# Optimization experiments

Measured on AMD Instinct MI355X. Metric: run time of the kernel, lower is better.

Reference implementation:

```python
import jax, jax.numpy as jnp
import numpy as np

B, H, NC, CS, D = 4, 16, 64, 64, 64
BASE_LR = 1.0
EPS = 1e-6


def setup_inputs() -> dict:
    key = jax.random.key(0)
    ks = jax.random.split(key, 4)
    xk = jax.random.normal(ks[0], (B, H, NC, CS, D), jnp.float32)
    xv = jax.random.normal(ks[1], (B, H, NC, CS, D), jnp.float32)
    # weights/theta use the module's N(0, 0.02) init scale
    weight = 0.02 * jax.random.normal(ks[2], (H, D, D), jnp.float32)
    bias = jnp.zeros((H, 1, D), jnp.float32)
    gamma = jnp.ones((H, 1, D), jnp.float32)
    beta = jnp.zeros((H, 1, D), jnp.float32)
    theta = 0.02 * jax.random.normal(ks[3], (H, D, 1), jnp.float32)
    theta_bias = jnp.zeros((H, 1, 1), jnp.float32)
    alpha = jnp.zeros((CS,), jnp.float32)
    return dict(xk=xk, xv=xv, weight=weight, bias=bias, gamma=gamma,
                beta=beta, theta=theta, theta_bias=theta_bias, alpha=alpha)


def _ttt(xk, xv, weight, bias, gamma, beta, theta, theta_bias, alpha):
    Bq, Hq, NCq, CSq, Dq = xk.shape
    # TTTDynamicLearningGate: token_idx = clamp(1/arange + alpha, 0)
    token_idx = jnp.maximum(1.0 / jnp.arange(1, CSq + 1, dtype=xk.dtype) + alpha, 0.0)
    token_eta = token_idx[None, None, :, None]  # [1,1,CS,1]
    g = gamma[None]       # [1,H,1,D]
    bt = beta[None]       # [1,H,1,D]
    tb = theta_bias[None]  # [1,H,1,1]
    # detach(): tile slow weights over batch -> fast weights
    W0 = jnp.broadcast_to(weight[None], (Bq, Hq, Dq, Dq))
    b0 = jnp.broadcast_to(bias[None], (Bq, Hq, 1, Dq))

    def step(carry, chunk):
        W, b = carry
        xk_c, xv_c = chunk  # [B,H,CS,D]
        # lr gate: eta = token_eta * (base_lr * sigmoid(x @ theta + b) / head_dim)
        lr = jax.nn.sigmoid(jnp.einsum('bhkc,hcd->bhkd', xk_c, theta) + tb)
        eta = token_eta * (BASE_LR * lr / Dq)  # [B,H,CS,1]
        # forward through fast weights (depth = 1)
        z = xk_c @ W + b
        # multi-head LayerNorm, detailed
        mu = z.mean(-1, keepdims=True)
        var = ((z - mu) ** 2).mean(-1, keepdims=True)
        std = jnp.sqrt(var + EPS)
        x_hat = (z - mu) / std
        y = g * x_hat + bt
        # L2 reconstruction grad through LN (manual backward)
        grad_out = y - (xv_c - xk_c)
        gxh = grad_out * g
        grad_x = (Dq * gxh - gxh.sum(-1, keepdims=True)
                  - x_hat * (gxh * x_hat).sum(-1, keepdims=True)) / (Dq * std)
        # fast-weight delta + step()
        dW = jnp.einsum('bhkd,bhke->bhde', eta * xk_c, grad_x)
        db = (eta * grad_x).sum(-2, keepdims=True)
        Wn, bn = W - dW, b - db
        return (Wn, bn), xk_c @ Wn + bn

    chunks = (jnp.moveaxis(xk, 2, 0), jnp.moveaxis(xv, 2, 0))  # [NC,B,H,CS,D]
    (_, _), outs = jax.lax.scan(step, (W0, b0), chunks)
    return jnp.moveaxis(outs, 0, 2)  # [B,H,NC,CS,D]


def reference(xk, xv, weight, bias, gamma, beta, theta, theta_bias, alpha):
    return _ttt(xk, xv, weight, bias, gamma, beta, theta, theta_bias, alpha)
```

## Files before the change

kernel.cpp:

```cpp
#include <hip/hip_runtime.h>
#include <hip/hip_bf16.h>
#include <math.h>

#define NCC 64
#define CSC 64
#define DC 64
#define S 72
#define SZ 68
#define EPSF 1e-6f
#define LDS_BYTES 82944

typedef __attribute__((ext_vector_type(8))) short bf16x8;
typedef __attribute__((ext_vector_type(4))) float f32x4;
typedef __attribute__((ext_vector_type(4))) short short4v;

static __device__ __forceinline__ short cvt_bf16(float x) {
    union { __hip_bfloat16 b; short s; } u;
    u.b = __float2bfloat16(x);
    return u.s;
}

#define DPP_ROR_ADD(v, N)                                                     \
    do {                                                                      \
        union { float f; int i; } _u, _r;                                     \
        _u.f = (v);                                                           \
        _r.i = __builtin_amdgcn_mov_dpp(_u.i, 0x120 + (N), 0xF, 0xF, true);   \
        (v) += _r.f;                                                          \
    } while (0)

static __device__ __forceinline__ float red16(float v) {
    DPP_ROR_ADD(v, 1);
    DPP_ROR_ADD(v, 2);
    DPP_ROR_ADD(v, 4);
    DPP_ROR_ADD(v, 8);
    return v;
}

__global__ __launch_bounds__(512, 1) void ttt_kernel(
    const float* __restrict__ xk, const float* __restrict__ xv,
    const float* __restrict__ weight, const float* __restrict__ bias,
    const float* __restrict__ gamma, const float* __restrict__ beta,
    const float* __restrict__ theta, const float* __restrict__ theta_bias,
    const float* __restrict__ alpha, float* __restrict__ out)
{
    extern __shared__ char sb[];
    auto xs_rm = (short (*)[CSC][S])(sb);
    auto xsT   = (short (*)[DC][S]) (sb + 18432);
    auto gsT   = (short (*)[S])     (sb + 36864);
    auto Gr    = (short (*)[S])     (sb + 46080);
    auto Wtb   = (short (*)[S])     (sb + 55296);
    auto zT    = (float (*)[SZ])    (sb + 64512);
    auto dbp   = (float (*)[DC])    (sb + 81920);

    const int t  = threadIdx.x;
    const int w  = t >> 6;
    const bool lo = (w < 4);
    const int ws = w & 3;
    const int l  = t & 63;
    const int g  = l >> 4, la = l & 15;
    const int r0 = 16*ws + 4*g;
    const int ts = 64*ws + l;
    const int bh = blockIdx.x;
    const int h  = bh & 15;

    const size_t bh_off = (size_t)bh * NCC*CSC*DC;
    const float* xkb = xk + bh_off;
    const float* xvb = xv + bh_off;
    float*       ob  = out + bh_off;

    float bcol[4];
#pragma unroll
    for (int n = 0; n < 4; ++n) bcol[n] = bias[h*DC + 16*n + la];

    float gam[4], bet[4], thv[4], tok[4], tb = 0.f;
    float Wreg[4][4];
    float xkg[4][4], xvg[4][4];
    float4 xl[4];
    float xkh[4][4];

    if (lo) {
#pragma unroll
        for (int n = 0; n < 4; ++n) {
            gam[n] = gamma[h*DC + 16*n + la];
            bet[n] = beta [h*DC + 16*n + la];
            thv[n] = theta[h*DC + 16*n + la];
        }
        tb = theta_bias[h];
#pragma unroll
        for (int i = 0; i < 4; ++i)
            tok[i] = fmaxf(1.0f/(float)(r0+i+1) + alpha[r0+i], 0.0f);
        const float* wg = weight + h*DC*DC;
#pragma unroll
        for (int i = 0; i < 4; ++i)
#pragma unroll
            for (int n = 0; n < 4; ++n)
                Wreg[i][n] = wg[(r0+i)*DC + 16*n + la];
#pragma unroll
        for (int n = 0; n < 4; ++n) {
            short4v sv;
#pragma unroll
            for (int i = 0; i < 4; ++i) sv[i] = cvt_bf16(Wreg[i][n]);
            *(short4v*)&Wtb[16*n + la][r0] = sv;
        }
#pragma unroll
        for (int i = 0; i < 4; ++i)
#pragma unroll
            for (int n = 0; n < 4; ++n) {
                xkg[i][n] = xkb[(r0+i)*DC + 16*n + la];
                xvg[i][n] = xvb[(r0+i)*DC + 16*n + la];
            }
    } else {
#pragma unroll
        for (int i4 = 0; i4 < 4; ++i4) xl[i4] = ((const float4*)xkb)[ts + 256*i4];
#pragma unroll
        for (int i = 0; i < 4; ++i)
#pragma unroll
            for (int n = 0; n < 4; ++n)
                xkh[i][n] = xkb[(r0+i)*DC + 16*n + la];
#pragma unroll
        for (int i4 = 0; i4 < 4; ++i4) {
            int f = ts + 256*i4, k = f >> 4, j = f & 15;
            short4v s4;
            s4[0]=cvt_bf16(xl[i4].x); s4[1]=cvt_bf16(xl[i4].y);
            s4[2]=cvt_bf16(xl[i4].z); s4[3]=cvt_bf16(xl[i4].w);
            *(short4v*)&xs_rm[0][k][4*j] = s4;
        }
#pragma unroll
        for (int n = 0; n < 4; ++n) {
            short4v sv;
#pragma unroll
            for (int i = 0; i < 4; ++i) sv[i] = cvt_bf16(xkh[i][n]);
            *(short4v*)&xsT[0][16*n + la][r0] = sv;
        }
    }
    __syncthreads();

    for (int c = 0; c < NCC; ++c) {
        const int cb = c & 1, nb = cb ^ 1;

        if (lo) {
            const bf16x8 a0 = *(const bf16x8*)&xs_rm[cb][16*ws + la][8*g];
            const bf16x8 a1 = *(const bf16x8*)&xs_rm[cb][16*ws + la][32 + 8*g];
            f32x4 zt[4];
#pragma unroll
            for (int n = 0; n < 4; ++n) {
                bf16x8 w0 = *(const bf16x8*)&Wtb[16*n + la][8*g];
                bf16x8 w1 = *(const bf16x8*)&Wtb[16*n + la][32 + 8*g];
                f32x4 zz = {0.f,0.f,0.f,0.f};
                zz = __builtin_amdgcn_mfma_f32_16x16x32_bf16(a0, w0, zz, 0,0,0);
                zz = __builtin_amdgcn_mfma_f32_16x16x32_bf16(a1, w1, zz, 0,0,0);
                zt[n] = zz;
                *(f32x4*)&zT[16*n + la][r0] = zz;
            }
            float gsv[4][4];
#pragma unroll
            for (int i = 0; i < 4; ++i) {
                float z0 = zt[0][i]+bcol[0], z1 = zt[1][i]+bcol[1];
                float z2 = zt[2][i]+bcol[2], z3 = zt[3][i]+bcol[3];
                float szz = red16(z0*z0 + z1*z1 + z2*z2 + z3*z3);
                float sz  = red16(z0 + z1 + z2 + z3);
                float thd = red16(xkg[i][0]*thv[0] + xkg[i][1]*thv[1] +
                                  xkg[i][2]*thv[2] + xkg[i][3]*thv[3]);
                float mu  = sz * (1.0f/DC);
                float var = szz*(1.0f/DC) - mu*mu;
                float rstd = rsqrtf(var + EPSF);
                float ex  = __expf(-(thd + tb));
                float lr  = __builtin_amdgcn_rcpf(1.0f + ex);
                float eta = tok[i]*lr*(1.0f/DC);
                float zz4[4] = {z0,z1,z2,z3};
                float xh[4], gxh[4], a1v = 0.f, a2v = 0.f;
#pragma unroll
                for (int n = 0; n < 4; ++n) {
                    xh[n] = (zz4[n]-mu)*rstd;
                    float y  = fmaf(gam[n], xh[n], bet[n]);
                    float go = y - xvg[i][n] + xkg[i][n];
                    gxh[n] = go*gam[n];
                    a1v += gxh[n];
                    a2v = fmaf(gxh[n], xh[n], a2v);
                }
                float s1 = red16(a1v), s2 = red16(a2v);
                float sc = rstd*(1.0f/DC)*eta;
#pragma unroll
                for (int n = 0; n < 4; ++n)
                    gsv[i][n] = (64.f*gxh[n] - s1 - xh[n]*s2)*sc;
            }
#pragma unroll
            for (int n = 0; n < 4; ++n) {
                short4v sg;
#pragma unroll
                for (int i = 0; i < 4; ++i) sg[i] = cvt_bf16(gsv[i][n]);
                *(short4v*)&gsT[16*n + la][r0] = sg;
            }
            float dbl[4];
#pragma unroll
            for (int n = 0; n < 4; ++n) {
                float dd = gsv[0][n]+gsv[1][n]+gsv[2][n]+gsv[3][n];
                dd += __shfl_xor(dd, 16);
                dd += __shfl_xor(dd, 32);
                dbl[n] = dd;
            }
            if (l < 16) {
                f32x4 dv = {dbl[0], dbl[1], dbl[2], dbl[3]};
                *(f32x4*)&dbp[ws][4*la] = dv;
            }
        } else {
            const bf16x8 a0 = *(const bf16x8*)&xs_rm[cb][16*ws + la][8*g];
            const bf16x8 a1 = *(const bf16x8*)&xs_rm[cb][16*ws + la][32 + 8*g];
#pragma unroll
            for (int n = 0; n < 4; ++n) {
                bf16x8 b0 = *(const bf16x8*)&xs_rm[cb][16*n + la][8*g];
                bf16x8 b1 = *(const bf16x8*)&xs_rm[cb][16*n + la][32 + 8*g];
                f32x4 cc = {0.f,0.f,0.f,0.f};
                cc = __builtin_amdgcn_mfma_f32_16x16x32_bf16(a0, b0, cc, 0,0,0);
                cc = __builtin_amdgcn_mfma_f32_16x16x32_bf16(a1, b1, cc, 0,0,0);
                short4v sg;
#pragma unroll
                for (int i = 0; i < 4; ++i) sg[i] = cvt_bf16(cc[i]);
                *(short4v*)&Gr[16*n + la][r0] = sg;
            }
            if (c + 1 < NCC) {
                const float* xkn = xkb + (c+1)*CSC*DC;
#pragma unroll
                for (int i4 = 0; i4 < 4; ++i4) xl[i4] = ((const float4*)xkn)[ts + 256*i4];
#pragma unroll
                for (int i = 0; i < 4; ++i)
#pragma unroll
                    for (int n = 0; n < 4; ++n)
                        xkh[i][n] = xkn[(r0+i)*DC + 16*n + la];
#pragma unroll
                for (int i4 = 0; i4 < 4; ++i4) {
                    int f = ts + 256*i4, k = f >> 4, j = f & 15;
                    short4v s4;
                    s4[0]=cvt_bf16(xl[i4].x); s4[1]=cvt_bf16(xl[i4].y);
                    s4[2]=cvt_bf16(xl[i4].z); s4[3]=cvt_bf16(xl[i4].w);
                    *(short4v*)&xs_rm[nb][k][4*j] = s4;
                }
#pragma unroll
                for (int n = 0; n < 4; ++n) {
                    short4v sv;
#pragma unroll
                    for (int i = 0; i < 4; ++i) sv[i] = cvt_bf16(xkh[i][n]);
                    *(short4v*)&xsT[nb][16*n + la][r0] = sv;
                }
            }
        }
        __syncthreads();

        {
            f32x4 d0v = *(const f32x4*)&dbp[0][4*la];
            f32x4 d1v = *(const f32x4*)&dbp[1][4*la];
            f32x4 d2v = *(const f32x4*)&dbp[2][4*la];
            f32x4 d3v = *(const f32x4*)&dbp[3][4*la];
#pragma unroll
            for (int n = 0; n < 4; ++n)
                bcol[n] -= d0v[n] + d1v[n] + d2v[n] + d3v[n];
        }

        if (lo) {
            const bf16x8 ax0 = *(const bf16x8*)&xsT[cb][16*ws + la][8*g];
            const bf16x8 ax1 = *(const bf16x8*)&xsT[cb][16*ws + la][32 + 8*g];
#pragma unroll
            for (int n = 0; n < 4; ++n) {
                bf16x8 q0 = *(const bf16x8*)&gsT[16*n + la][8*g];
                bf16x8 q1 = *(const bf16x8*)&gsT[16*n + la][32 + 8*g];
                f32x4 dw = {0.f,0.f,0.f,0.f};
                dw = __builtin_amdgcn_mfma_f32_16x16x32_bf16(ax0, q0, dw, 0,0,0);
                dw = __builtin_amdgcn_mfma_f32_16x16x32_bf16(ax1, q1, dw, 0,0,0);
                short4v sw;
#pragma unroll
                for (int i = 0; i < 4; ++i) {
                    Wreg[i][n] -= dw[i];
                    sw[i] = cvt_bf16(Wreg[i][n]);
                }
                *(short4v*)&Wtb[16*n + la][r0] = sw;
            }
            if (c + 1 < NCC) {
                const float* xkn = xkb + (c+1)*CSC*DC;
                const float* xvn = xvb + (c+1)*CSC*DC;
#pragma unroll
                for (int i = 0; i < 4; ++i)
#pragma unroll
                    for (int n = 0; n < 4; ++n) {
                        xkg[i][n] = xkn[(r0+i)*DC + 16*n + la];
                        xvg[i][n] = xvn[(r0+i)*DC + 16*n + la];
                    }
            }
        } else {
            const bf16x8 ar0 = *(const bf16x8*)&Gr[16*ws + la][8*g];
            const bf16x8 ar1 = *(const bf16x8*)&Gr[16*ws + la][32 + 8*g];
            float* oc = ob + c*CSC*DC;
#pragma unroll
            for (int n = 0; n < 4; ++n) {
                bf16x8 q0 = *(const bf16x8*)&gsT[16*n + la][8*g];
                bf16x8 q1 = *(const bf16x8*)&gsT[16*n + la][32 + 8*g];
                f32x4 og = {0.f,0.f,0.f,0.f};
                og = __builtin_amdgcn_mfma_f32_16x16x32_bf16(ar0, q0, og, 0,0,0);
                og = __builtin_amdgcn_mfma_f32_16x16x32_bf16(ar1, q1, og, 0,0,0);
                f32x4 zv = *(const f32x4*)&zT[16*n + la][r0];
#pragma unroll
                for (int i = 0; i < 4; ++i)
                    oc[(r0+i)*DC + 16*n + la] = zv[i] - og[i] + bcol[n];
            }
        }
        __syncthreads();
    }
}

extern "C" void kernel_launch(void* const* d_in, const int* in_sizes, int n_in,
                              void* d_out, int out_size, void* d_ws, size_t ws_size,
                              hipStream_t stream) {
    const float* xk         = (const float*)d_in[0];
    const float* xv         = (const float*)d_in[1];
    const float* weight     = (const float*)d_in[2];
    const float* bias       = (const float*)d_in[3];
    const float* gamma      = (const float*)d_in[4];
    const float* beta       = (const float*)d_in[5];
    const float* theta      = (const float*)d_in[6];
    const float* theta_bias = (const float*)d_in[7];
    const float* alpha      = (const float*)d_in[8];
    float* out = (float*)d_out;

    (void)hipFuncSetAttribute((const void*)ttt_kernel,
                              hipFuncAttributeMaxDynamicSharedMemorySize,
                              LDS_BYTES);
    ttt_kernel<<<64, 512, LDS_BYTES, stream>>>(xk, xv, weight, bias, gamma, beta,
                                               theta, theta_bias, alpha, out);
}
```

Baseline: 145.0 us.

## Split LayerNorm-gradient work across all eight waves and drop zT LDS staging

Both wave groups now compute z = xk·W redundantly, and each wave handles two of the four rows per lane group for the LayerNorm backward and lr-gate math, which halves per-wave serial VALU work. The hi waves keep z in registers for the output instead of reading it from an LDS zT buffer. xk for the gate is now read from the bf16 LDS copy rather than fp32 global loads, and prefetch duties are redistributed. This costs duplicated MFMAs, an 8-way bias reduction, and reduced precision in the gate and residual xk term.

Result: no change. 145.7 us (+0.4%).

```diff
diff --git a/kernel.cpp b/kernel.cpp
--- a/kernel.cpp
+++ b/kernel.cpp
@@ -6,18 +6,22 @@
 #define CSC 64
 #define DC 64
 #define S 72
-#define SZ 68
 #define EPSF 1e-6f
-#define LDS_BYTES 82944
+#define LDS_BYTES 66560
 
 typedef __attribute__((ext_vector_type(8))) short bf16x8;
 typedef __attribute__((ext_vector_type(4))) float f32x4;
 typedef __attribute__((ext_vector_type(4))) short short4v;
+typedef __attribute__((ext_vector_type(2))) short short2v;
 
 static __device__ __forceinline__ short cvt_bf16(float x) {
     union { __hip_bfloat16 b; short s; } u;
     u.b = __float2bfloat16(x);
     return u.s;
+}
+static __device__ __forceinline__ float bf16_to_f(unsigned hw) {
+    union { unsigned u; float f; } v; v.u = hw << 16;
+    return v.f;
 }
 
 #define DPP_ROR_ADD(v, N)                                                     \
@@ -49,46 +53,53 @@
     auto gsT   = (short (*)[S])     (sb + 36864);
     auto Gr    = (short (*)[S])     (sb + 46080);
     auto Wtb   = (short (*)[S])     (sb + 55296);
-    auto zT    = (float (*)[SZ])    (sb + 64512);
-    auto dbp   = (float (*)[DC])    (sb + 81920);
-
-    const int t  = threadIdx.x;
-    const int w  = t >> 6;
+    auto dbp   = (float (*)[DC])    (sb + 64512);
+
+    const int t   = threadIdx.x;
+    const int w   = t >> 6;
     const bool lo = (w < 4);
-    const int ws = w & 3;
-    const int l  = t & 63;
-    const int g  = l >> 4, la = l & 15;
-    const int r0 = 16*ws + 4*g;
-    const int ts = 64*ws + l;
-    const int bh = blockIdx.x;
-    const int h  = bh & 15;
+    const int ws  = w & 3;
+    const int l   = t & 63;
+    const int g   = l >> 4, la = l & 15;
+    const int r0  = 16*ws + 4*g;
+    const int io  = lo ? 0 : 2;
+    const int ts  = 64*ws + l;
+    const int bh  = blockIdx.x;
+    const int h   = bh & 15;
 
     const size_t bh_off = (size_t)bh * NCC*CSC*DC;
     const float* xkb = xk + bh_off;
     const float* xvb = xv + bh_off;
     float*       ob  = out + bh_off;
 
-    float bcol[4];
-#pragma unroll
-    for (int n = 0; n < 4; ++n) bcol[n] = bias[h*DC + 16*n + la];
-
-    float gam[4], bet[4], thv[4], tok[4], tb = 0.f;
+    float gam[4], bet[4], thv[4], bcol[4];
+#pragma unroll
+    for (int n = 0; n < 4; ++n) {
+        gam[n]  = gamma[h*DC + 16*n + la];
+        bet[n]  = beta [h*DC + 16*n + la];
+        thv[n]  = theta[h*DC + 16*n + la];
+        bcol[n] = bias [h*DC + 16*n + la];
+    }
+    const float tb = theta_bias[h];
+    float tokk[2];
+#pragma unroll
+    for (int ii = 0; ii < 2; ++ii) {
+        int r = r0 + io + ii;
+        tokk[ii] = fmaxf(1.0f/(float)(r+1) + alpha[r], 0.0f);
+    }
+
     float Wreg[4][4];
-    float xkg[4][4], xvg[4][4];
     float4 xl[4];
     float xkh[4][4];
+    float xvg[2][4];
+
+#pragma unroll
+    for (int ii = 0; ii < 2; ++ii)
+#pragma unroll
+        for (int n = 0; n < 4; ++n)
+            xvg[ii][n] = xvb[(r0+io+ii)*DC + 16*n + la];
 
     if (lo) {
-#pragma unroll
-        for (int n = 0; n < 4; ++n) {
-            gam[n] = gamma[h*DC + 16*n + la];
-            bet[n] = beta [h*DC + 16*n + la];
-            thv[n] = theta[h*DC + 16*n + la];
-        }
-        tb = theta_bias[h];
-#pragma unroll
-        for (int i = 0; i < 4; ++i)
-            tok[i] = fmaxf(1.0f/(float)(r0+i+1) + alpha[r0+i], 0.0f);
         const float* wg = weight + h*DC*DC;
 #pragma unroll
         for (int i = 0; i < 4; ++i)
@@ -102,14 +113,6 @@
             for (int i = 0; i < 4; ++i) sv[i] = cvt_bf16(Wreg[i][n]);
             *(short4v*)&Wtb[16*n + la][r0] = sv;
         }
-#pragma unroll
-        for (int i = 0; i < 4; ++i)
-#pragma unroll
-            for (int n = 0; n < 4; ++n) {
-                xkg[i][n] = xkb[(r0+i)*DC + 16*n + la];
-                xvg[i][n] = xvb[(r0+i)*DC + 16*n + la];
-            }
-    } else {
 #pragma unroll
         for (int i4 = 0; i4 < 4; ++i4) xl[i4] = ((const float4*)xkb)[ts + 256*i4];
 #pragma unroll
@@ -137,75 +140,21 @@
 
     for (int c = 0; c < NCC; ++c) {
         const int cb = c & 1, nb = cb ^ 1;
-
-        if (lo) {
-            const bf16x8 a0 = *(const bf16x8*)&xs_rm[cb][16*ws + la][8*g];
-            const bf16x8 a1 = *(const bf16x8*)&xs_rm[cb][16*ws + la][32 + 8*g];
-            f32x4 zt[4];
-#pragma unroll
-            for (int n = 0; n < 4; ++n) {
-                bf16x8 w0 = *(const bf16x8*)&Wtb[16*n + la][8*g];
-                bf16x8 w1 = *(const bf16x8*)&Wtb[16*n + la][32 + 8*g];
-                f32x4 zz = {0.f,0.f,0.f,0.f};
-                zz = __builtin_amdgcn_mfma_f32_16x16x32_bf16(a0, w0, zz, 0,0,0);
-                zz = __builtin_amdgcn_mfma_f32_16x16x32_bf16(a1, w1, zz, 0,0,0);
-                zt[n] = zz;
-                *(f32x4*)&zT[16*n + la][r0] = zz;
-            }
-            float gsv[4][4];
-#pragma unroll
-            for (int i = 0; i < 4; ++i) {
-                float z0 = zt[0][i]+bcol[0], z1 = zt[1][i]+bcol[1];
-                float z2 = zt[2][i]+bcol[2], z3 = zt[3][i]+bcol[3];
-                float szz = red16(z0*z0 + z1*z1 + z2*z2 + z3*z3);
-                float sz  = red16(z0 + z1 + z2 + z3);
-                float thd = red16(xkg[i][0]*thv[0] + xkg[i][1]*thv[1] +
-                                  xkg[i][2]*thv[2] + xkg[i][3]*thv[3]);
-                float mu  = sz * (1.0f/DC);
-                float var = szz*(1.0f/DC) - mu*mu;
-                float rstd = rsqrtf(var + EPSF);
-                float ex  = __expf(-(thd + tb));
-                float lr  = __builtin_amdgcn_rcpf(1.0f + ex);
-                float eta = tok[i]*lr*(1.0f/DC);
-                float zz4[4] = {z0,z1,z2,z3};
-                float xh[4], gxh[4], a1v = 0.f, a2v = 0.f;
-#pragma unroll
-                for (int n = 0; n < 4; ++n) {
-                    xh[n] = (zz4[n]-mu)*rstd;
-                    float y  = fmaf(gam[n], xh[n], bet[n]);
-                    float go = y - xvg[i][n] + xkg[i][n];
-                    gxh[n] = go*gam[n];
-                    a1v += gxh[n];
-                    a2v = fmaf(gxh[n], xh[n], a2v);
-                }
-                float s1 = red16(a1v), s2 = red16(a2v);
-                float sc = rstd*(1.0f/DC)*eta;
-#pragma unroll
-                for (int n = 0; n < 4; ++n)
-                    gsv[i][n] = (64.f*gxh[n] - s1 - xh[n]*s2)*sc;
-            }
-#pragma unroll
-            for (int n = 0; n < 4; ++n) {
-                short4v sg;
-#pragma unroll
-                for (int i = 0; i < 4; ++i) sg[i] = cvt_bf16(gsv[i][n]);
-                *(short4v*)&gsT[16*n + la][r0] = sg;
-            }
-            float dbl[4];
-#pragma unroll
-            for (int n = 0; n < 4; ++n) {
-                float dd = gsv[0][n]+gsv[1][n]+gsv[2][n]+gsv[3][n];
-                dd += __shfl_xor(dd, 16);
-                dd += __shfl_xor(dd, 32);
-                dbl[n] = dd;
-            }
-            if (l < 16) {
-                f32x4 dv = {dbl[0], dbl[1], dbl[2], dbl[3]};
-                *(f32x4*)&dbp[ws][4*la] = dv;
-            }
-        } else {
-            const bf16x8 a0 = *(const bf16x8*)&xs_rm[cb][16*ws + la][8*g];
-            const bf16x8 a1 = *(const bf16x8*)&xs_rm[cb][16*ws + la][32 + 8*g];
+        const bool pf = (c + 1 < NCC);
+
+        const bf16x8 a0 = *(const bf16x8*)&xs_rm[cb][16*ws + la][8*g];
+        const bf16x8 a1 = *(const bf16x8*)&xs_rm[cb][16*ws + la][32 + 8*g];
+        f32x4 zt[4];
+#pragma unroll
+        for (int n = 0; n < 4; ++n) {
+            bf16x8 w0 = *(const bf16x8*)&Wtb[16*n + la][8*g];
+            bf16x8 w1 = *(const bf16x8*)&Wtb[16*n + la][32 + 8*g];
+            f32x4 zz = {0.f,0.f,0.f,0.f};
+            zz = __builtin_amdgcn_mfma_f32_16x16x32_bf16(a0, w0, zz, 0,0,0);
+            zz = __builtin_amdgcn_mfma_f32_16x16x32_bf16(a1, w1, zz, 0,0,0);
+            zt[n] = zz;
+        }
+        if (!lo) {
 #pragma unroll
             for (int n = 0; n < 4; ++n) {
                 bf16x8 b0 = *(const bf16x8*)&xs_rm[cb][16*n + la][8*g];
@@ -218,7 +167,25 @@
                 for (int i = 0; i < 4; ++i) sg[i] = cvt_bf16(cc[i]);
                 *(short4v*)&Gr[16*n + la][r0] = sg;
             }
-            if (c + 1 < NCC) {
+        }
+
+        float xkq[2][4];
+#pragma unroll
+        for (int n = 0; n < 4; ++n) {
+            unsigned pk = *(const unsigned*)&xsT[cb][16*n + la][r0 + io];
+            xkq[0][n] = bf16_to_f(pk & 0xFFFFu);
+            xkq[1][n] = bf16_to_f(pk >> 16);
+        }
+
+        float xvN[2][4];
+        if (pf) {
+            const float* xvn = xvb + (c+1)*CSC*DC;
+#pragma unroll
+            for (int ii = 0; ii < 2; ++ii)
+#pragma unroll
+                for (int n = 0; n < 4; ++n)
+                    xvN[ii][n] = xvn[(r0+io+ii)*DC + 16*n + la];
+            if (lo) {
                 const float* xkn = xkb + (c+1)*CSC*DC;
 #pragma unroll
                 for (int i4 = 0; i4 < 4; ++i4) xl[i4] = ((const float4*)xkn)[ts + 256*i4];
@@ -227,6 +194,102 @@
 #pragma unroll
                     for (int n = 0; n < 4; ++n)
                         xkh[i][n] = xkn[(r0+i)*DC + 16*n + la];
+            }
+        }
+
+        float zrow[2][4];
+        if (lo) {
+#pragma unroll
+            for (int n = 0; n < 4; ++n) { zrow[0][n] = zt[n][0]; zrow[1][n] = zt[n][1]; }
+        } else {
+#pragma unroll
+            for (int n = 0; n < 4; ++n) { zrow[0][n] = zt[n][2]; zrow[1][n] = zt[n][3]; }
+        }
+
+        float gsv[2][4];
+#pragma unroll
+        for (int ii = 0; ii < 2; ++ii) {
+            float z4[4];
+#pragma unroll
+            for (int n = 0; n < 4; ++n) z4[n] = zrow[ii][n] + bcol[n];
+            float szz = red16(z4[0]*z4[0] + z4[1]*z4[1] + z4[2]*z4[2] + z4[3]*z4[3]);
+            float sz  = red16(z4[0] + z4[1] + z4[2] + z4[3]);
+            float thd = red16(xkq[ii][0]*thv[0] + xkq[ii][1]*thv[1] +
+                              xkq[ii][2]*thv[2] + xkq[ii][3]*thv[3]);
+            float mu   = sz * (1.0f/DC);
+            float var  = szz*(1.0f/DC) - mu*mu;
+            float rstd = rsqrtf(var + EPSF);
+            float ex   = __expf(-(thd + tb));
+            float lr   = __builtin_amdgcn_rcpf(1.0f + ex);
+            float eta  = tokk[ii]*lr*(1.0f/DC);
+            float xh[4], gxh[4], a1v = 0.f, a2v = 0.f;
+#pragma unroll
+            for (int n = 0; n < 4; ++n) {
+                xh[n] = (z4[n]-mu)*rstd;
+                float y  = fmaf(gam[n], xh[n], bet[n]);
+                float go = y - xvg[ii][n] + xkq[ii][n];
+                gxh[n] = go*gam[n];
+                a1v += gxh[n];
+                a2v = fmaf(gxh[n], xh[n], a2v);
+            }
+            float s1 = red16(a1v), s2 = red16(a2v);
+            float sc = rstd*(1.0f/DC)*eta;
+#pragma unroll
+            for (int n = 0; n < 4; ++n)
+                gsv[ii][n] = (64.f*gxh[n] - s1 - xh[n]*s2)*sc;
+        }
+#pragma unroll
+        for (int n = 0; n < 4; ++n) {
+            short2v sg;
+            sg[0] = cvt_bf16(gsv[0][n]);
+            sg[1] = cvt_bf16(gsv[1][n]);
+            *(short2v*)&gsT[16*n + la][r0 + io] = sg;
+        }
+        float dbl[4];
+#pragma unroll
+        for (int n = 0; n < 4; ++n) {
+            float dd = gsv[0][n] + gsv[1][n];
+            dd += __shfl_xor(dd, 16);
+            dd += __shfl_xor(dd, 32);
+            dbl[n] = dd;
+        }
+        if (l < 16) {
+            f32x4 dv = {dbl[0], dbl[1], dbl[2], dbl[3]};
+            *(f32x4*)&dbp[w][4*la] = dv;
+        }
+        __syncthreads();
+
+        {
+            f32x4 s = *(const f32x4*)&dbp[0][4*la];
+#pragma unroll
+            for (int p = 1; p < 8; ++p) {
+                f32x4 d = *(const f32x4*)&dbp[p][4*la];
+#pragma unroll
+                for (int n = 0; n < 4; ++n) s[n] += d[n];
+            }
+#pragma unroll
+            for (int n = 0; n < 4; ++n) bcol[n] -= s[n];
+        }
+
+        if (lo) {
+            const bf16x8 ax0 = *(const bf16x8*)&xsT[cb][16*ws + la][8*g];
+            const bf16x8 ax1 = *(const bf16x8*)&xsT[cb][16*ws + la][32 + 8*g];
+#pragma unroll
+            for (int n = 0; n < 4; ++n) {
+                bf16x8 q0 = *(const bf16x8*)&gsT[16*n + la][8*g];
+                bf16x8 q1 = *(const bf16x8*)&gsT[16*n + la][32 + 8*g];
+                f32x4 dw = {0.f,0.f,0.f,0.f};
+                dw = __builtin_amdgcn_mfma_f32_16x16x32_bf16(ax0, q0, dw, 0,0,0);
+                dw = __builtin_amdgcn_mfma_f32_16x16x32_bf16(ax1, q1, dw, 0,0,0);
+                short4v sw;
+#pragma unroll
+                for (int i = 0; i < 4; ++i) {
+                    Wreg[i][n] -= dw[i];
+                    sw[i] = cvt_bf16(Wreg[i][n]);
+                }
+                *(short4v*)&Wtb[16*n + la][r0] = sw;
+            }
+            if (pf) {
 #pragma unroll
                 for (int i4 = 0; i4 < 4; ++i4) {
                     int f = ts + 256*i4, k = f >> 4, j = f & 15;
@@ -243,48 +306,6 @@
                     *(short4v*)&xsT[nb][16*n + la][r0] = sv;
                 }
             }
-        }
-        __syncthreads();
-
-        {
-            f32x4 d0v = *(const f32x4*)&dbp[0][4*la];
-            f32x4 d1v = *(const f32x4*)&dbp[1][4*la];
-            f32x4 d2v = *(const f32x4*)&dbp[2][4*la];
-            f32x4 d3v = *(const f32x4*)&dbp[3][4*la];
-#pragma unroll
-            for (int n = 0; n < 4; ++n)
-                bcol[n] -= d0v[n] + d1v[n] + d2v[n] + d3v[n];
-        }
-
-        if (lo) {
-            const bf16x8 ax0 = *(const bf16x8*)&xsT[cb][16*ws + la][8*g];
-            const bf16x8 ax1 = *(const bf16x8*)&xsT[cb][16*ws + la][32 + 8*g];
-#pragma unroll
-            for (int n = 0; n < 4; ++n) {
-                bf16x8 q0 = *(const bf16x8*)&gsT[16*n + la][8*g];
-                bf16x8 q1 = *(const bf16x8*)&gsT[16*n + la][32 + 8*g];
-                f32x4 dw = {0.f,0.f,0.f,0.f};
-                dw = __builtin_amdgcn_mfma_f32_16x16x32_bf16(ax0, q0, dw, 0,0,0);
-                dw = __builtin_amdgcn_mfma_f32_16x16x32_bf16(ax1, q1, dw, 0,0,0);
-                short4v sw;
-#pragma unroll
-                for (int i = 0; i < 4; ++i) {
-                    Wreg[i][n] -= dw[i];
-                    sw[i] = cvt_bf16(Wreg[i][n]);
-                }
-                *(short4v*)&Wtb[16*n + la][r0] = sw;
-            }
-            if (c + 1 < NCC) {
-                const float* xkn = xkb + (c+1)*CSC*DC;
-                const float* xvn = xvb + (c+1)*CSC*DC;
-#pragma unroll
-                for (int i = 0; i < 4; ++i)
-#pragma unroll
-                    for (int n = 0; n < 4; ++n) {
-                        xkg[i][n] = xkn[(r0+i)*DC + 16*n + la];
-                        xvg[i][n] = xvn[(r0+i)*DC + 16*n + la];
-                    }
-            }
         } else {
             const bf16x8 ar0 = *(const bf16x8*)&Gr[16*ws + la][8*g];
             const bf16x8 ar1 = *(const bf16x8*)&Gr[16*ws + la][32 + 8*g];
@@ -296,11 +317,17 @@
                 f32x4 og = {0.f,0.f,0.f,0.f};
                 og = __builtin_amdgcn_mfma_f32_16x16x32_bf16(ar0, q0, og, 0,0,0);
                 og = __builtin_amdgcn_mfma_f32_16x16x32_bf16(ar1, q1, og, 0,0,0);
-                f32x4 zv = *(const f32x4*)&zT[16*n + la][r0];
 #pragma unroll
                 for (int i = 0; i < 4; ++i)
-                    oc[(r0+i)*DC + 16*n + la] = zv[i] - og[i] + bcol[n];
-            }
+                    oc[(r0+i)*DC + 16*n + la] = zt[n][i] - og[i] + bcol[n];
+            }
+        }
+        if (pf) {
+#pragma unroll
+            for (int ii = 0; ii < 2; ++ii)
+#pragma unroll
+                for (int n = 0; n < 4; ++n)
+                    xvg[ii][n] = xvN[ii][n];
         }
         __syncthreads();
     }
```
